# Kernel tuning notes

Hardware: AMD Instinct MI355X
Metric: run time of the kernel (lower is better)

## Reference

```python
import jax, jax.numpy as jnp
import numpy as np

H = 128          # LSTMCell hidden size (fixed in module)
D_IN = 128       # input_dim
D_PROJ = 256     # input_layer output / LSTM input size
LAYER_NUM = 2
DA = 128
R = 8
OUT_DIM = 7
B = 256
T = 512
TS = 32          # time_steps


def _lstm_cell(h, c, x_t, W_ih, b_ih, W_hh, b_hh):
    # PyTorch LSTMCell gate order: i, f, g, o
    gates = x_t @ W_ih.T + h @ W_hh.T + (b_ih + b_hh)
    i, f, g, o = jnp.split(gates, 4, axis=-1)
    c_new = jax.nn.sigmoid(f) * c + jax.nn.sigmoid(i) * jnp.tanh(g)
    h_new = jax.nn.sigmoid(o) * jnp.tanh(c_new)
    return h_new, c_new


def _chunked_lstm(x_tbd, W_ih, b_ih, W_hh, b_hh, w_time, time_steps):
    # x_tbd: [T, B, 256]. Every `time_steps` steps, h/c are replaced by a
    # learned linear reweighting (time_w_layer) of the buffered chunk states;
    # the chunk's last emitted output is the reweighted h (as in the source).
    Tt, Bb, Dd = x_tbd.shape

    def cell_step(carry, x_t):
        h, c = carry
        h, c = _lstm_cell(h, c, x_t, W_ih, b_ih, W_hh, b_hh)
        return (h, c), (h, c)

    def chunk_step(carry, x_chunk):        # x_chunk: [ts, B, 256]
        _, (hs, cs) = jax.lax.scan(cell_step, carry, x_chunk)  # hs: [ts, B, H]
        h_new = jnp.einsum('t,tbh->bh', w_time, hs)
        c_new = jnp.einsum('t,tbh->bh', w_time, cs)
        return (h_new, c_new), hs.at[-1].set(h_new)

    n_chunks = Tt // time_steps
    x_chunks = x_tbd.reshape(n_chunks, time_steps, Bb, Dd)
    h0 = jnp.zeros((Bb, H), x_tbd.dtype)
    _, outs = jax.lax.scan(chunk_step, (h0, jnp.zeros_like(h0)), x_chunks)
    return outs.reshape(Tt, Bb, H)


def setup_inputs() -> dict:
    key = jax.random.key(0)
    ks = jax.random.split(key, 16)
    def unif(k, shape, fan_in):
        bound = 1.0 / np.sqrt(fan_in)
        return jax.random.uniform(k, shape, jnp.float32, -bound, bound)
    inp = {
        'x': jax.random.normal(ks[0], (B, T, D_IN), jnp.float32),
        'W_in': unif(ks[1], (D_PROJ, D_IN), D_IN),
        'b_in': unif(ks[2], (D_PROJ,), D_IN),
        'W_ih': unif(ks[3], (4 * H, D_PROJ), H),
        'b_ih': unif(ks[4], (4 * H,), H),
        'W_hh': unif(ks[5], (4 * H, H), H),
        'b_hh': unif(ks[6], (4 * H,), H),
        'w_time': unif(ks[7], (TS,), TS),
        'W_a1': unif(ks[8], (DA, 2 * H), 2 * H),
        'b_a1': unif(ks[9], (DA,), 2 * H),
        'W_a2': unif(ks[10], (R, DA), DA),
        'W_out': unif(ks[11], (OUT_DIM, 2 * H * R), 2 * H * R),
        'b_out': unif(ks[12], (OUT_DIM,), 2 * H * R),
        'length': jax.random.randint(ks[13], (B,), T // 2, T + 1),
        'batch_size': B,
        'time_steps': TS,
        'r': R,
    }
    return inp


def reference(x, W_in, b_in, W_ih, b_ih, W_hh, b_hh, w_time, W_a1, b_a1,
              W_a2, W_out, b_out, length, batch_size, time_steps, r):
    Bb, Tt, _ = x.shape
    out = x @ W_in.T + b_in                       # [B, T, 256]
    for _ in range(LAYER_NUM):                    # shared LSTM weights per source
        inp = jnp.transpose(out, (1, 0, 2))       # [T, B, 256]
        out1 = _chunked_lstm(inp, W_ih, b_ih, W_hh, b_hh, w_time, time_steps)
        out2 = _chunked_lstm(inp[::-1], W_ih, b_ih, W_hh, b_hh, w_time, time_steps)
        # NOTE: backward outputs are NOT re-reversed (faithful to source)
        out = jnp.transpose(jnp.concatenate([out1, out2], axis=-1), (1, 0, 2))
    # attention (dropout = identity at eval)
    pot = jnp.tanh(out @ W_a1.T + b_a1) @ W_a2.T  # [B, T, r]
    mask = (jnp.arange(Tt)[None, :] < length[:, None])[:, :, None]
    logits = jnp.where(mask, pot, -jnp.inf)
    weight = jnp.where(mask, jax.nn.softmax(logits, axis=1), 0.0)  # [B, T, r]
    wT = jnp.transpose(weight, (0, 2, 1))          # [B, r, T]
    pooled = jnp.einsum('brt,bth->brh', wT, out).reshape(Bb, -1)   # [B, r*256]
    out_final = jax.nn.log_softmax(pooled @ W_out.T + b_out, axis=1)
    sw = jnp.sqrt(wT)
    gram = jnp.einsum('brt,bst->brs', sw, sw)      # [B, r, r]
    penalty = jnp.sum((gram - 1.0) ** 2)           # oneMat is all-ones
    return out_final, penalty
```

## Files before the change

### kernel.cpp

```cpp
#include <hip/hip_runtime.h>
#include <math.h>

namespace {

constexpr int Bb = 256, Tt = 512, Dp = 256, Hh = 128, G = 512;
constexpr int M = Tt * Bb;

typedef __attribute__((ext_vector_type(8))) short short8v;
typedef __attribute__((ext_vector_type(4))) float f32x4;

__device__ __forceinline__ float sigf(float x) {
  return __builtin_amdgcn_rcpf(1.0f + __expf(-x));
}
__device__ __forceinline__ float tanhfast(float x) {
  const float e = __expf(2.0f * x);
  return 1.0f - 2.0f * __builtin_amdgcn_rcpf(e + 1.0f);
}
__device__ __forceinline__ float b2f(unsigned short u) {
  return __uint_as_float((unsigned int)u << 16);
}
__device__ __forceinline__ unsigned short f2b(float f) {
  unsigned int u = __float_as_uint(f);
  u += 0x7FFFu + ((u >> 16) & 1u);
  return (unsigned short)(u >> 16);
}
__device__ __forceinline__ unsigned int pack2(float a, float b) {
  return (unsigned int)f2b(a) | ((unsigned int)f2b(b) << 16);
}
__device__ __forceinline__ void gload16(const unsigned short* g, unsigned short* l) {
  __builtin_amdgcn_global_load_lds(
      (const __attribute__((address_space(1))) unsigned int*)g,
      (__attribute__((address_space(3))) unsigned int*)l, 16, 0, 0);
}
__device__ __forceinline__ void block_sync_lds() {
  __builtin_amdgcn_sched_barrier(0);
  asm volatile("s_waitcnt lgkmcnt(0)" ::: "memory");
  __builtin_amdgcn_s_barrier();
  __builtin_amdgcn_sched_barrier(0);
}

__global__ __launch_bounds__(256) void wconv_k(const float* __restrict__ src,
                                               unsigned short* __restrict__ dst) {
  const int i = (blockIdx.x * 256 + threadIdx.x) * 4;
  const float4 v = *reinterpret_cast<const float4*>(src + i);
  uint2 o; o.x = pack2(v.x, v.y); o.y = pack2(v.z, v.w);
  *reinterpret_cast<uint2*>(dst + i) = o;
}

__global__ __launch_bounds__(256) void xconv_k(const float* __restrict__ x,
                                               unsigned short* __restrict__ out) {
  const int tid = threadIdx.x;
  const int m = blockIdx.x * 8 + (tid >> 5);
  const int t = m >> 8, b = m & 255;
  const int c4 = (tid & 31) * 4;
  const float4 v = *reinterpret_cast<const float4*>(x + ((size_t)b * Tt + t) * 128 + c4);
  uint2 o; o.x = pack2(v.x, v.y); o.y = pack2(v.z, v.w);
  *reinterpret_cast<uint2*>(out + (size_t)m * 128 + c4) = o;
}

template<int K, int POT, typename CT>
__global__ __launch_bounds__(256) void mgemm_k(const unsigned short* __restrict__ A,
    const unsigned short* __restrict__ W, const float* __restrict__ bias1,
    const float* __restrict__ bias2, const float* __restrict__ Wa2,
    CT* __restrict__ C, int N) {
  constexpr int NK = K / 64;
  __shared__ unsigned short smem[32768];
  unsigned short* aLds = smem;
  unsigned short* wLds = smem + 16384;
  const int tid = threadIdx.x;
  const int lane = tid & 63;
  const int wave = tid >> 6;
  const int wm = wave >> 1, wn = wave & 1;
  const int m0 = blockIdx.y * 128, n0 = blockIdx.x * 128;
  const int lrow = lane & 15, lk8 = (lane >> 4) * 8;

  const unsigned short* Ab = A + (size_t)(m0 + lrow) * K + lk8;
  const unsigned short* Wb = W + (size_t)(n0 + lrow) * K + lk8;

  auto stage = [&](int buf, int kb) {
#pragma unroll
    for (int i = 0; i < 4; ++i) {
      const int c = wave * 4 + i, f = c & 7, kc = c >> 3;
      const size_t go = (size_t)(f * 16) * K + kb * 64 + kc * 32;
      gload16(Ab + go, &aLds[buf * 8192 + c * 512]);
      gload16(Wb + go, &wLds[buf * 8192 + c * 512]);
    }
  };

  f32x4 acc[4][4] = {};
  stage(0, 0);
  __syncthreads();
  int cur = 0;
  for (int kb = 0; kb < NK; ++kb) {
    if (kb + 1 < NK) stage(cur ^ 1, kb + 1);
#pragma unroll
    for (int kc = 0; kc < 2; ++kc) {
      short8v af[4], bfr[4];
#pragma unroll
      for (int i = 0; i < 4; ++i)
        af[i] = *reinterpret_cast<const short8v*>(
            &aLds[cur * 8192 + ((kc * 8 + wm * 4 + i) * 64 + lane) * 8]);
#pragma unroll
      for (int j = 0; j < 4; ++j)
        bfr[j] = *reinterpret_cast<const short8v*>(
            &wLds[cur * 8192 + ((kc * 8 + wn * 4 + j) * 64 + lane) * 8]);
#pragma unroll
      for (int i = 0; i < 4; ++i)
#pragma unroll
        for (int j = 0; j < 4; ++j)
          acc[i][j] = __builtin_amdgcn_mfma_f32_16x16x32_bf16(af[i], bfr[j], acc[i][j], 0, 0, 0);
    }
    __syncthreads();
    cur ^= 1;
  }

  if constexpr (POT) {
    unsigned short* pt = smem;
#pragma unroll
    for (int j = 0; j < 4; ++j) {
      const int coln = wn * 64 + j * 16 + (lane & 15);
      const float bv = bias1[coln];
#pragma unroll
      for (int i = 0; i < 4; ++i) {
        const int rown = wm * 64 + i * 16 + ((lane >> 4) << 2);
#pragma unroll
        for (int r = 0; r < 4; ++r)
          pt[(rown + r) * 136 + coln] = f2b(tanhfast(acc[i][j][r] + bv));
      }
    }
    __syncthreads();
    short8v wfr[4];
#pragma unroll
    for (int ks = 0; ks < 4; ++ks) {
      short8v f = {0, 0, 0, 0, 0, 0, 0, 0};
      if (lrow < 8) {
        const float* src = Wa2 + lrow * 128 + ks * 32 + lk8;
        const float4 a = *reinterpret_cast<const float4*>(src);
        const float4 b = *reinterpret_cast<const float4*>(src + 4);
        f[0] = (short)f2b(a.x); f[1] = (short)f2b(a.y);
        f[2] = (short)f2b(a.z); f[3] = (short)f2b(a.w);
        f[4] = (short)f2b(b.x); f[5] = (short)f2b(b.y);
        f[6] = (short)f2b(b.z); f[7] = (short)f2b(b.w);
      }
      wfr[ks] = f;
    }
    float* pot = reinterpret_cast<float*>(C);
#pragma unroll
    for (int ff = 0; ff < 2; ++ff) {
      const int fr = wave * 2 + ff;
      f32x4 pacc = {0.f, 0.f, 0.f, 0.f};
#pragma unroll
      for (int ks = 0; ks < 4; ++ks) {
        const short8v af = *reinterpret_cast<const short8v*>(
            &pt[(fr * 16 + lrow) * 136 + ks * 32 + lk8]);
        pacc = __builtin_amdgcn_mfma_f32_16x16x32_bf16(af, wfr[ks], pacc, 0, 0, 0);
      }
      if ((lane & 15) < 8) {
#pragma unroll
        for (int r = 0; r < 4; ++r)
          pot[(size_t)(m0 + fr * 16 + ((lane >> 4) << 2) + r) * 8 + (lane & 15)] = pacc[r];
      }
    }
  } else {
#pragma unroll
    for (int j = 0; j < 4; ++j) {
      const int gn = n0 + wn * 64 + j * 16 + (lane & 15);
      float bv = bias1[gn];
      if (bias2) bv += bias2[gn];
#pragma unroll
      for (int i = 0; i < 4; ++i) {
        const int gmb = m0 + wm * 64 + i * 16 + ((lane >> 4) << 2);
#pragma unroll
        for (int r = 0; r < 4; ++r) {
          const float v = acc[i][j][r] + bv;
          const size_t oidx = (size_t)(gmb + r) * N + gn;
          if constexpr (sizeof(CT) == 2) C[oidx] = f2b(v); else C[oidx] = v;
        }
      }
    }
  }
}

__global__ __launch_bounds__(512, 2) void lstm_k(const unsigned short* __restrict__ P,
    const float* __restrict__ Whh, const float* __restrict__ wtime,
    unsigned short* __restrict__ Y) {
  const int tid = threadIdx.x;
  const int lane = tid & 63;
  const int w = tid >> 6;
  const int u = lane & 15;
  const int q = lane >> 4;
  const int dir = blockIdx.x >> 7;
  const int b0 = (blockIdx.x & 127) * 2;

  __shared__ unsigned short hbuf[2][2048];
  __shared__ unsigned short histb[4096];
  __shared__ float wts[32];

  short8v bfrag[4][4];
#pragma unroll
  for (int gt = 0; gt < 4; ++gt) {
    const int col = gt * 128 + w * 16 + u;
#pragma unroll
    for (int ks = 0; ks < 4; ++ks) {
      const int k0 = ks * 32 + q * 8;
      const float4 w0 = *reinterpret_cast<const float4*>(Whh + (size_t)col * 128 + k0);
      const float4 w1 = *reinterpret_cast<const float4*>(Whh + (size_t)col * 128 + k0 + 4);
      short8v f;
      f[0] = (short)f2b(w0.x); f[1] = (short)f2b(w0.y);
      f[2] = (short)f2b(w0.z); f[3] = (short)f2b(w0.w);
      f[4] = (short)f2b(w1.x); f[5] = (short)f2b(w1.y);
      f[6] = (short)f2b(w1.z); f[7] = (short)f2b(w1.w);
      bfrag[gt][ks] = f;
    }
  }

  for (int i = tid; i < 2048; i += 512) { hbuf[0][i] = 0; hbuf[1][i] = 0; }
  if (tid < 32) wts[tid] = wtime[tid];

  const int r_own = q & 1;
  const int colh = w * 16 + u;
  const unsigned short* pb = P + (size_t)(b0 + r_own) * G + colh;
  const ptrdiff_t pstep = (dir ? -(ptrdiff_t)1 : (ptrdiff_t)1) * (ptrdiff_t)Bb * G;
  ptrdiff_t ptoff = (ptrdiff_t)((size_t)(dir ? (Tt - 1) : 0) * Bb * G);
  unsigned short pg0[4], pg1[4], pg2[4];
  if (lane < 32) {
#pragma unroll
    for (int gt = 0; gt < 4; ++gt) {
      pg0[gt] = pb[ptoff + gt * 128];
      pg1[gt] = pb[ptoff + pstep + gt * 128];
      pg2[gt] = pb[ptoff + 2 * pstep + gt * 128];
    }
  }
  ptoff += 3 * pstep;
  float c_st = 0.f, ha = 0.f, ca = 0.f;
  __syncthreads();

  auto body = [&](int s, int cur) {
    unsigned short npg[4] = {0, 0, 0, 0};
    if (lane < 32 && s < Tt - 3) {
#pragma unroll
      for (int gt = 0; gt < 4; ++gt) npg[gt] = pb[ptoff + gt * 128];
    }
    short8v afrag[4];
#pragma unroll
    for (int ks = 0; ks < 4; ++ks)
      afrag[ks] = *reinterpret_cast<const short8v*>(&hbuf[cur][(ks * 4 + q) * 128 + u * 8]);
    f32x4 gacc[4];
#pragma unroll
    for (int gt = 0; gt < 4; ++gt) {
      f32x4 acc = {0.f, 0.f, 0.f, 0.f};
#pragma unroll
      for (int ks = 0; ks < 4; ++ks)
        acc = __builtin_amdgcn_mfma_f32_16x16x32_bf16(afrag[ks], bfrag[gt][ks], acc, 0, 0, 0);
      gacc[gt] = acc;
    }
    if (lane < 32) {
      const float wt = wts[s & 31];
      float g4[4];
#pragma unroll
      for (int gt = 0; gt < 4; ++gt) g4[gt] = gacc[gt][0] + b2f(pg0[gt]);
      float cs = sigf(g4[1]) * c_st + sigf(g4[0]) * tanhfast(g4[2]);
      float hn = sigf(g4[3]) * tanhfast(cs);
      ha += wt * hn;
      ca += wt * cs;
      if ((s & 31) == 31) { hn = ha; cs = ca; ha = 0.f; ca = 0.f; }
      c_st = cs;
      const unsigned short hb = f2b(hn);
      hbuf[cur ^ 1][(colh >> 3) * 128 + r_own * 32 + (colh & 7)] = hb;
      histb[((s & 15) * 2 + r_own) * 128 + colh] = hb;
    }
    if ((s & 7) == 0 && s) {
      const int k = tid >> 6, r2 = (tid >> 5) & 1, c4 = (tid & 31) * 4;
      const int bs = s - 8;
      const uint2 v = *reinterpret_cast<const uint2*>(
          &histb[(((bs + k) & 15) * 2 + r2) * 128 + c4]);
      *reinterpret_cast<uint2*>(
          &Y[((size_t)(bs + k) * Bb + b0 + r2) * Dp + dir * Hh + c4]) = v;
    }
    block_sync_lds();
#pragma unroll
    for (int gt = 0; gt < 4; ++gt) {
      pg0[gt] = pg1[gt]; pg1[gt] = pg2[gt]; pg2[gt] = npg[gt];
    }
    ptoff += pstep;
  };

  for (int s = 0; s < Tt; s += 2) {
    body(s, 0);
    body(s + 1, 1);
  }
  {
    const int k = tid >> 6, r2 = (tid >> 5) & 1, c4 = (tid & 31) * 4;
    const int bs = Tt - 8;
    const uint2 v = *reinterpret_cast<const uint2*>(
        &histb[(((bs + k) & 15) * 2 + r2) * 128 + c4]);
    *reinterpret_cast<uint2*>(
        &Y[((size_t)(bs + k) * Bb + b0 + r2) * Dp + dir * Hh + c4]) = v;
  }
}

__global__ __launch_bounds__(256) void softmax_k(const float* __restrict__ pot,
    const int* __restrict__ length, float* __restrict__ Wt) {
  const int b = blockIdx.x >> 3, r = blockIdx.x & 7;
  const int tid = threadIdx.x;
  const int len = length[b];
  __shared__ float rbuf[4];
  const int t1 = tid, t2 = tid + 256;
  const float x1 = (t1 < len) ? pot[((size_t)t1 * Bb + b) * 8 + r] : -INFINITY;
  const float x2 = (t2 < len) ? pot[((size_t)t2 * Bb + b) * 8 + r] : -INFINITY;
  float m = fmaxf(x1, x2);
#pragma unroll
  for (int off = 32; off >= 1; off >>= 1) m = fmaxf(m, __shfl_xor(m, off));
  if ((tid & 63) == 0) rbuf[tid >> 6] = m;
  __syncthreads();
  m = fmaxf(fmaxf(rbuf[0], rbuf[1]), fmaxf(rbuf[2], rbuf[3]));
  const float e1 = (t1 < len) ? __expf(x1 - m) : 0.f;
  const float e2 = (t2 < len) ? __expf(x2 - m) : 0.f;
  float ssum = e1 + e2;
#pragma unroll
  for (int off = 32; off >= 1; off >>= 1) ssum += __shfl_xor(ssum, off);
  __syncthreads();
  if ((tid & 63) == 0) rbuf[tid >> 6] = ssum;
  __syncthreads();
  ssum = rbuf[0] + rbuf[1] + rbuf[2] + rbuf[3];
  const float inv = 1.0f / ssum;
  float* wrow = Wt + ((size_t)b * 8 + r) * Tt;
  wrow[t1] = e1 * inv;
  wrow[t2] = e2 * inv;
}

__global__ __launch_bounds__(256) void pool_k(const unsigned short* __restrict__ Y,
    const float* __restrict__ Wt, const float* __restrict__ Wout,
    const float* __restrict__ bout, float* __restrict__ outF,
    float* __restrict__ penpart) {
  const int b = blockIdx.x;
  const int tid = threadIdx.x;
  __shared__ float ws[8 * 513];
  __shared__ float pooled[2048];
  __shared__ float red[256];
  __shared__ float lg[8];
  for (int i = tid; i < 4096; i += 256) ws[(i >> 9) * 513 + (i & 511)] = Wt[(size_t)b * 4096 + i];
  __syncthreads();
  float acc[8] = {};
  for (int t = 0; t < Tt; ++t) {
    const float y = b2f(Y[((size_t)t * Bb + b) * Dp + tid]);
#pragma unroll
    for (int r = 0; r < 8; ++r) acc[r] += ws[r * 513 + t] * y;
  }
#pragma unroll
  for (int r = 0; r < 8; ++r) pooled[r * 256 + tid] = acc[r];
  __syncthreads();
  for (int o = 0; o < 7; ++o) {
    float p = 0.f;
    for (int j = tid; j < 2048; j += 256) p += pooled[j] * Wout[(size_t)o * 2048 + j];
    red[tid] = p;
    __syncthreads();
    for (int st = 128; st >= 1; st >>= 1) {
      if (tid < st) red[tid] += red[tid + st];
      __syncthreads();
    }
    if (tid == 0) lg[o] = red[0] + bout[o];
    __syncthreads();
  }
  if (tid == 0) {
    float mx = lg[0];
    for (int o = 1; o < 7; ++o) mx = fmaxf(mx, lg[o]);
    float ssum = 0.f;
    for (int o = 0; o < 7; ++o) ssum += __expf(lg[o] - mx);
    const float lse = mx + __logf(ssum);
    for (int o = 0; o < 7; ++o) outF[b * 7 + o] = lg[o] - lse;
  }
  for (int i = tid; i < 4096; i += 256) {
    const int rr = i >> 9, t = i & 511;
    ws[rr * 513 + t] = sqrtf(ws[rr * 513 + t]);
  }
  __syncthreads();
  float pp = 0.f;
  if (tid < 64) {
    const int rr = tid >> 3, ssi = tid & 7;
    float g = 0.f;
    for (int t = 0; t < Tt; ++t) g += ws[rr * 513 + t] * ws[ssi * 513 + t];
    const float d = g - 1.0f;
    pp = d * d;
  }
  red[tid] = pp;
  __syncthreads();
  for (int st = 128; st >= 1; st >>= 1) {
    if (tid < st) red[tid] += red[tid + st];
    __syncthreads();
  }
  if (tid == 0) penpart[b] = red[0];
}

__global__ __launch_bounds__(256) void penred_k(const float* __restrict__ penpart,
                                                float* __restrict__ outp) {
  const int tid = threadIdx.x;
  __shared__ float red[256];
  red[tid] = penpart[tid];
  __syncthreads();
  for (int st = 128; st >= 1; st >>= 1) {
    if (tid < st) red[tid] += red[tid + st];
    __syncthreads();
  }
  if (tid == 0) outp[0] = red[0];
}

}

extern "C" void kernel_launch(void* const* d_in, const int* in_sizes, int n_in,
                              void* d_out, int out_size, void* d_ws, size_t ws_size,
                              hipStream_t stream) {
  (void)in_sizes; (void)n_in; (void)out_size;
  const float* x     = (const float*)d_in[0];
  const float* W_in  = (const float*)d_in[1];
  const float* b_in  = (const float*)d_in[2];
  const float* W_ih  = (const float*)d_in[3];
  const float* b_ih  = (const float*)d_in[4];
  const float* W_hh  = (const float*)d_in[5];
  const float* b_hh  = (const float*)d_in[6];
  const float* wtime = (const float*)d_in[7];
  const float* W_a1  = (const float*)d_in[8];
  const float* b_a1  = (const float*)d_in[9];
  const float* W_a2  = (const float*)d_in[10];
  const float* W_out = (const float*)d_in[11];
  const float* b_out = (const float*)d_in[12];
  const int*   length= (const int*)d_in[13];
  float* outF = (float*)d_out;

  typedef unsigned short bf16;
  char* ws = (char*)d_ws;
  size_t off = 0;
  auto alloc = [&](size_t bytes) {
    void* p = ws + off; off += (bytes + 255) & ~(size_t)255; return p;
  };
  bf16*  act  = (bf16*)alloc((size_t)M * 256 * 2);
  bf16*  Pg   = (bf16*)alloc((size_t)M * 512 * 2);
  bf16*  xb   = (bf16*)alloc((size_t)M * 128 * 2);
  float* pot  = (float*)alloc((size_t)M * 8 * 4);
  float* Wt   = (float*)alloc((size_t)Bb * 8 * Tt * 4);
  float* penp = (float*)alloc(Bb * 4);
  bf16*  Wihb = (bf16*)alloc(512 * 256 * 2);
  bf16*  Winb = (bf16*)alloc(256 * 128 * 2);
  bf16*  Wa1b = (bf16*)alloc(128 * 256 * 2);

  if (ws_size < off) return;

  const dim3 blk(256);
  wconv_k<<<dim3(32),  blk, 0, stream>>>(W_in, Winb);
  wconv_k<<<dim3(128), blk, 0, stream>>>(W_ih, Wihb);
  wconv_k<<<dim3(32),  blk, 0, stream>>>(W_a1, Wa1b);
  xconv_k<<<dim3(M / 8), blk, 0, stream>>>(x, xb);
  mgemm_k<128, 0, bf16><<<dim3(2, M / 128), blk, 0, stream>>>(xb, Winb, b_in, nullptr, nullptr, act, 256);
  mgemm_k<256, 0, bf16><<<dim3(4, M / 128), blk, 0, stream>>>(act, Wihb, b_ih, b_hh, nullptr, Pg, 512);
  lstm_k<<<dim3(256), dim3(512), 0, stream>>>(Pg, W_hh, wtime, act);
  mgemm_k<256, 0, bf16><<<dim3(4, M / 128), blk, 0, stream>>>(act, Wihb, b_ih, b_hh, nullptr, Pg, 512);
  lstm_k<<<dim3(256), dim3(512), 0, stream>>>(Pg, W_hh, wtime, act);
  mgemm_k<256, 1, float><<<dim3(1, M / 128), blk, 0, stream>>>(act, Wa1b, b_a1, nullptr, W_a2, pot, 128);
  softmax_k<<<dim3(Bb * 8), blk, 0, stream>>>(pot, length, Wt);
  pool_k<<<dim3(Bb), blk, 0, stream>>>(act, Wt, W_out, b_out, outF, penp);
  penred_k<<<dim3(1), blk, 0, stream>>>(penp, outF + Bb * 7);
}
```

Measured before the change: 929.2 us.

## Interleave forward and backward LSTM directions in one block with skewed pipelining

Each LSTM block now handles both directions for its batch pair, alternating MFMA for one direction with the gate nonlinearities of the other, which is skewed by one step. Gate preactivations are prefetched as 32-bit words into shared-memory double buffers instead of per-lane 16-bit global loads. The aim is to hide the serial MFMA-to-activation latency of one recurrence behind the other's work and to halve the block count (128 blocks at one block per CU). The cost is two barriers per step, more shared memory, and a longer per-block serial chain.

```diff
diff --git a/kernel.cpp b/kernel.cpp
--- a/kernel.cpp
+++ b/kernel.cpp
@@ -181,7 +181,7 @@
   }
 }
 
-__global__ __launch_bounds__(512, 2) void lstm_k(const unsigned short* __restrict__ P,
+__global__ __launch_bounds__(512, 1) void lstm_k(const unsigned short* __restrict__ P,
     const float* __restrict__ Whh, const float* __restrict__ wtime,
     unsigned short* __restrict__ Y) {
   const int tid = threadIdx.x;
@@ -189,11 +189,11 @@
   const int w = tid >> 6;
   const int u = lane & 15;
   const int q = lane >> 4;
-  const int dir = blockIdx.x >> 7;
-  const int b0 = (blockIdx.x & 127) * 2;
-
-  __shared__ unsigned short hbuf[2][2048];
-  __shared__ unsigned short histb[4096];
+  const int b0 = blockIdx.x * 2;
+
+  __shared__ unsigned short hbufA[2048], hbufB[2048];
+  __shared__ unsigned int pgA[2][512], pgB[2][512];
+  __shared__ unsigned short histA[4096], histB[4096];
   __shared__ float wts[32];
 
   short8v bfrag[4][4];
@@ -214,88 +214,154 @@
     }
   }
 
-  for (int i = tid; i < 2048; i += 512) { hbuf[0][i] = 0; hbuf[1][i] = 0; }
+  for (int i = tid; i < 2048; i += 512) { hbufA[i] = 0; hbufB[i] = 0; }
   if (tid < 32) wts[tid] = wtime[tid];
+  const unsigned int* P32 = reinterpret_cast<const unsigned int*>(P);
+  const size_t bstep = (size_t)Bb * 256;
+  const size_t word = (size_t)(b0 + (tid >> 8)) * 256 + (tid & 255);
+  pgA[0][tid] = P32[word];
+  unsigned int hA1 = P32[bstep + word];
+  unsigned int hA2 = P32[2 * bstep + word];
+  pgB[1][tid] = P32[(size_t)(Tt - 1) * bstep + word];
+  unsigned int hB1 = P32[(size_t)(Tt - 2) * bstep + word];
+  unsigned int hB2 = P32[(size_t)(Tt - 3) * bstep + word];
+  size_t poffA = 3 * bstep + word;
+  size_t poffB = (size_t)(Tt - 4) * bstep + word;
 
   const int r_own = q & 1;
   const int colh = w * 16 + u;
-  const unsigned short* pb = P + (size_t)(b0 + r_own) * G + colh;
-  const ptrdiff_t pstep = (dir ? -(ptrdiff_t)1 : (ptrdiff_t)1) * (ptrdiff_t)Bb * G;
-  ptrdiff_t ptoff = (ptrdiff_t)((size_t)(dir ? (Tt - 1) : 0) * Bb * G);
-  unsigned short pg0[4], pg1[4], pg2[4];
-  if (lane < 32) {
-#pragma unroll
-    for (int gt = 0; gt < 4; ++gt) {
-      pg0[gt] = pb[ptoff + gt * 128];
-      pg1[gt] = pb[ptoff + pstep + gt * 128];
-      pg2[gt] = pb[ptoff + 2 * pstep + gt * 128];
-    }
-  }
-  ptoff += 3 * pstep;
-  float c_st = 0.f, ha = 0.f, ca = 0.f;
-  __syncthreads();
-
-  auto body = [&](int s, int cur) {
-    unsigned short npg[4] = {0, 0, 0, 0};
-    if (lane < 32 && s < Tt - 3) {
-#pragma unroll
-      for (int gt = 0; gt < 4; ++gt) npg[gt] = pb[ptoff + gt * 128];
-    }
-    short8v afrag[4];
+  float cA = 0.f, haA = 0.f, caA = 0.f;
+  float cB = 0.f, haB = 0.f, caB = 0.f;
+  f32x4 gB[4];
+  __syncthreads();
+
+  auto body = [&](int s, int par) {
+    unsigned int nA = 0;
+    if (s + 3 < Tt) nA = P32[poffA];
+    short8v af[4];
 #pragma unroll
     for (int ks = 0; ks < 4; ++ks)
-      afrag[ks] = *reinterpret_cast<const short8v*>(&hbuf[cur][(ks * 4 + q) * 128 + u * 8]);
-    f32x4 gacc[4];
+      af[ks] = *reinterpret_cast<const short8v*>(&hbufA[(ks * 4 + q) * 128 + u * 8]);
+    f32x4 gA[4];
 #pragma unroll
     for (int gt = 0; gt < 4; ++gt) {
       f32x4 acc = {0.f, 0.f, 0.f, 0.f};
 #pragma unroll
       for (int ks = 0; ks < 4; ++ks)
-        acc = __builtin_amdgcn_mfma_f32_16x16x32_bf16(afrag[ks], bfrag[gt][ks], acc, 0, 0, 0);
-      gacc[gt] = acc;
-    }
-    if (lane < 32) {
-      const float wt = wts[s & 31];
+        acc = __builtin_amdgcn_mfma_f32_16x16x32_bf16(af[ks], bfrag[gt][ks], acc, 0, 0, 0);
+      gA[gt] = acc;
+    }
+    if (s < Tt - 1) pgA[par ^ 1][tid] = hA1;
+    if (s > 0 && lane < 32) {
+      const int sb = s - 1;
+      const float wt = wts[sb & 31];
       float g4[4];
 #pragma unroll
-      for (int gt = 0; gt < 4; ++gt) g4[gt] = gacc[gt][0] + b2f(pg0[gt]);
-      float cs = sigf(g4[1]) * c_st + sigf(g4[0]) * tanhfast(g4[2]);
+      for (int gt = 0; gt < 4; ++gt) {
+        const unsigned int pw = pgB[par][r_own * 256 + gt * 64 + (colh >> 1)];
+        const unsigned short pb = (colh & 1) ? (unsigned short)(pw >> 16)
+                                             : (unsigned short)(pw & 0xFFFF);
+        g4[gt] = gB[gt][0] + b2f(pb);
+      }
+      float cs = sigf(g4[1]) * cB + sigf(g4[0]) * tanhfast(g4[2]);
       float hn = sigf(g4[3]) * tanhfast(cs);
-      ha += wt * hn;
-      ca += wt * cs;
-      if ((s & 31) == 31) { hn = ha; cs = ca; ha = 0.f; ca = 0.f; }
-      c_st = cs;
+      haB += wt * hn; caB += wt * cs;
+      if ((sb & 31) == 31) { hn = haB; cs = caB; haB = 0.f; caB = 0.f; }
+      cB = cs;
       const unsigned short hb = f2b(hn);
-      hbuf[cur ^ 1][(colh >> 3) * 128 + r_own * 32 + (colh & 7)] = hb;
-      histb[((s & 15) * 2 + r_own) * 128 + colh] = hb;
+      hbufB[(colh >> 3) * 128 + r_own * 32 + (colh & 7)] = hb;
+      histB[((sb & 15) * 2 + r_own) * 128 + colh] = hb;
     }
     if ((s & 7) == 0 && s) {
       const int k = tid >> 6, r2 = (tid >> 5) & 1, c4 = (tid & 31) * 4;
       const int bs = s - 8;
       const uint2 v = *reinterpret_cast<const uint2*>(
-          &histb[(((bs + k) & 15) * 2 + r2) * 128 + c4]);
+          &histA[(((bs + k) & 15) * 2 + r2) * 128 + c4]);
       *reinterpret_cast<uint2*>(
-          &Y[((size_t)(bs + k) * Bb + b0 + r2) * Dp + dir * Hh + c4]) = v;
+          &Y[((size_t)(bs + k) * Bb + b0 + r2) * Dp + c4]) = v;
     }
     block_sync_lds();
+    hA1 = hA2; hA2 = nA; poffA += bstep;
+
+    unsigned int nB = 0;
+    if (s + 3 < Tt) nB = P32[poffB];
+#pragma unroll
+    for (int ks = 0; ks < 4; ++ks)
+      af[ks] = *reinterpret_cast<const short8v*>(&hbufB[(ks * 4 + q) * 128 + u * 8]);
 #pragma unroll
     for (int gt = 0; gt < 4; ++gt) {
-      pg0[gt] = pg1[gt]; pg1[gt] = pg2[gt]; pg2[gt] = npg[gt];
-    }
-    ptoff += pstep;
+      f32x4 acc = {0.f, 0.f, 0.f, 0.f};
+#pragma unroll
+      for (int ks = 0; ks < 4; ++ks)
+        acc = __builtin_amdgcn_mfma_f32_16x16x32_bf16(af[ks], bfrag[gt][ks], acc, 0, 0, 0);
+      gB[gt] = acc;
+    }
+    if (s < Tt - 1) pgB[par][tid] = hB1;
+    if (lane < 32) {
+      const float wt = wts[s & 31];
+      float g4[4];
+#pragma unroll
+      for (int gt = 0; gt < 4; ++gt) {
+        const unsigned int pw = pgA[par][r_own * 256 + gt * 64 + (colh >> 1)];
+        const unsigned short pb = (colh & 1) ? (unsigned short)(pw >> 16)
+                                             : (unsigned short)(pw & 0xFFFF);
+        g4[gt] = gA[gt][0] + b2f(pb);
+      }
+      float cs = sigf(g4[1]) * cA + sigf(g4[0]) * tanhfast(g4[2]);
+      float hn = sigf(g4[3]) * tanhfast(cs);
+      haA += wt * hn; caA += wt * cs;
+      if ((s & 31) == 31) { hn = haA; cs = caA; haA = 0.f; caA = 0.f; }
+      cA = cs;
+      const unsigned short hb = f2b(hn);
+      hbufA[(colh >> 3) * 128 + r_own * 32 + (colh & 7)] = hb;
+      histA[((s & 15) * 2 + r_own) * 128 + colh] = hb;
+    }
+    if ((s & 7) == 0 && s) {
+      const int k = tid >> 6, r2 = (tid >> 5) & 1, c4 = (tid & 31) * 4;
+      const int bs = s - 8;
+      const uint2 v = *reinterpret_cast<const uint2*>(
+          &histB[(((bs + k) & 15) * 2 + r2) * 128 + c4]);
+      *reinterpret_cast<uint2*>(
+          &Y[((size_t)(bs + k) * Bb + b0 + r2) * Dp + Hh + c4]) = v;
+    }
+    block_sync_lds();
+    hB1 = hB2; hB2 = nB; poffB -= bstep;
   };
 
   for (int s = 0; s < Tt; s += 2) {
     body(s, 0);
     body(s + 1, 1);
   }
+  if (lane < 32) {
+    const int sb = Tt - 1;
+    const float wt = wts[sb & 31];
+    float g4[4];
+#pragma unroll
+    for (int gt = 0; gt < 4; ++gt) {
+      const unsigned int pw = pgB[0][r_own * 256 + gt * 64 + (colh >> 1)];
+      const unsigned short pb = (colh & 1) ? (unsigned short)(pw >> 16)
+                                           : (unsigned short)(pw & 0xFFFF);
+      g4[gt] = gB[gt][0] + b2f(pb);
+    }
+    float cs = sigf(g4[1]) * cB + sigf(g4[0]) * tanhfast(g4[2]);
+    float hn = sigf(g4[3]) * tanhfast(cs);
+    haB += wt * hn;
+    if ((sb & 31) == 31) hn = haB;
+    const unsigned short hb = f2b(hn);
+    histB[((sb & 15) * 2 + r_own) * 128 + colh] = hb;
+  }
+  __syncthreads();
   {
     const int k = tid >> 6, r2 = (tid >> 5) & 1, c4 = (tid & 31) * 4;
     const int bs = Tt - 8;
-    const uint2 v = *reinterpret_cast<const uint2*>(
-        &histb[(((bs + k) & 15) * 2 + r2) * 128 + c4]);
+    const uint2 va = *reinterpret_cast<const uint2*>(
+        &histA[(((bs + k) & 15) * 2 + r2) * 128 + c4]);
     *reinterpret_cast<uint2*>(
-        &Y[((size_t)(bs + k) * Bb + b0 + r2) * Dp + dir * Hh + c4]) = v;
+        &Y[((size_t)(bs + k) * Bb + b0 + r2) * Dp + c4]) = va;
+    const uint2 vb = *reinterpret_cast<const uint2*>(
+        &histB[(((bs + k) & 15) * 2 + r2) * 128 + c4]);
+    *reinterpret_cast<uint2*>(
+        &Y[((size_t)(bs + k) * Bb + b0 + r2) * Dp + Hh + c4]) = vb;
   }
 }
 
@@ -452,9 +518,9 @@
   xconv_k<<<dim3(M / 8), blk, 0, stream>>>(x, xb);
   mgemm_k<128, 0, bf16><<<dim3(2, M / 128), blk, 0, stream>>>(xb, Winb, b_in, nullptr, nullptr, act, 256);
   mgemm_k<256, 0, bf16><<<dim3(4, M / 128), blk, 0, stream>>>(act, Wihb, b_ih, b_hh, nullptr, Pg, 512);
-  lstm_k<<<dim3(256), dim3(512), 0, stream>>>(Pg, W_hh, wtime, act);
+  lstm_k<<<dim3(128), dim3(512), 0, stream>>>(Pg, W_hh, wtime, act);
   mgemm_k<256, 0, bf16><<<dim3(4, M / 128), blk, 0, stream>>>(act, Wihb, b_ih, b_hh, nullptr, Pg, 512);
-  lstm_k<<<dim3(256), dim3(512), 0, stream>>>(Pg, W_hh, wtime, act);
+  lstm_k<<<dim3(128), dim3(512), 0, stream>>>(Pg, W_hh, wtime, act);
   mgemm_k<256, 1, float><<<dim3(1, M / 128), blk, 0, stream>>>(act, Wa1b, b_a1, nullptr, W_a2, pot, 128);
   softmax_k<<<dim3(Bb * 8), blk, 0, stream>>>(pot, length, Wt);
   pool_k<<<dim3(Bb), blk, 0, stream>>>(act, Wt, W_out, b_out, outF, penp);
```

Result: slower. 1.414 ms (+52.2%).
